# Kernel optimization log

Measured on AMD Instinct MI355X. Metric: run time of the kernel, lower is better.

The kernel has to match this reference:

```python
import jax, jax.numpy as jnp
import numpy as np

N = 100000      # nodes
E = 1600000     # edges (before self-loops)
F_IN = 512      # input features
H = 8           # heads layer 1
D = 8           # per-head dim layer 1
C = 40          # classes (layer 2 out, heads=1)
NEG_SLOPE = 0.2 # PyG GATConv default negative_slope


def setup_inputs() -> dict:
    key = jax.random.key(0)
    ks = jax.random.split(key, 10)
    x = jax.random.normal(ks[0], (N, F_IN), jnp.float32)
    edge_index = jax.random.randint(ks[1], (2, E), 0, N, dtype=jnp.int32)
    W1 = jax.random.normal(ks[2], (F_IN, H * D), jnp.float32) / np.float32(np.sqrt(F_IN))
    att_src1 = jax.random.normal(ks[3], (H, D), jnp.float32) / np.float32(np.sqrt(D))
    att_dst1 = jax.random.normal(ks[4], (H, D), jnp.float32) / np.float32(np.sqrt(D))
    b1 = jnp.zeros((H * D,), jnp.float32)
    W2 = jax.random.normal(ks[5], (H * D, C), jnp.float32) / np.float32(np.sqrt(H * D))
    att_src2 = jax.random.normal(ks[6], (1, C), jnp.float32) / np.float32(np.sqrt(C))
    att_dst2 = jax.random.normal(ks[7], (1, C), jnp.float32) / np.float32(np.sqrt(C))
    b2 = jnp.zeros((C,), jnp.float32)
    return {"x": x, "edge_index": edge_index, "W1": W1, "att_src1": att_src1,
            "att_dst1": att_dst1, "b1": b1, "W2": W2, "att_src2": att_src2,
            "att_dst2": att_dst2, "b2": b2}


def _gat_layer(x, src, dst, W, a_src, a_dst, heads, dim):
    # Dense projection, then per-head attention logits.
    h = (x @ W).reshape(-1, heads, dim)            # [N, H, D]
    alpha_s = jnp.einsum('nhd,hd->nh', h, a_src)   # [N, H]
    alpha_d = jnp.einsum('nhd,hd->nh', h, a_dst)
    e = jax.nn.leaky_relu(alpha_s[src] + alpha_d[dst], NEG_SLOPE)  # [E, H]
    # Segment softmax over edges grouped by destination node.
    emax = jax.ops.segment_max(e, dst, num_segments=N)
    emax = jnp.where(jnp.isfinite(emax), emax, 0.0)
    ee = jnp.exp(e - emax[dst])
    denom = jax.ops.segment_sum(ee, dst, num_segments=N)
    alpha = ee / (denom[dst] + 1e-16)              # [E, H]
    # Scatter-aggregate weighted neighbor features.
    msg = h[src] * alpha[:, :, None]               # [E, H, D]
    return jax.ops.segment_sum(msg, dst, num_segments=N)  # [N, H, D]


def reference(x, edge_index, W1, att_src1, att_dst1, b1, W2, att_src2, att_dst2, b2):
    # PyG GATConv adds self-loops by default.
    loops = jnp.arange(N, dtype=edge_index.dtype)
    src = jnp.concatenate([edge_index[0], loops])
    dst = jnp.concatenate([edge_index[1], loops])
    # Layer 1: 8 heads, concat=True, then ELU. (dropouts identity in eval mode)
    h1 = _gat_layer(x, src, dst, W1, att_src1, att_dst1, H, D).reshape(N, H * D) + b1
    h1 = jax.nn.elu(h1)
    # Layer 2: 1 head, concat=False -> mean over heads (trivial for H=1).
    h2 = _gat_layer(h1, src, dst, W2, att_src2, att_dst2, 1, C)[:, 0, :] + b2
    return jax.nn.log_softmax(h2, axis=1)
```

## Files before the change

kernel.cpp:

```cpp
#include <hip/hip_runtime.h>

#define F_IN   512
#define HD     64
#define NHEAD  8
#define NC     40
#define NEG    0.2f

typedef __attribute__((ext_vector_type(8))) short bf16x8;
typedef __attribute__((ext_vector_type(4))) float f32x4;

__device__ __forceinline__ float lrelu(float x) { return x > 0.0f ? x : NEG * x; }

__device__ __forceinline__ short f2bf(float f) {
    unsigned u = __float_as_uint(f);
    u += 0x7FFF + ((u >> 16) & 1);
    return (short)(u >> 16);
}
__device__ __forceinline__ float bf2f(short h) {
    return __uint_as_float(((unsigned)(unsigned short)h) << 16);
}
__device__ __forceinline__ float bfl(unsigned u) { return __uint_as_float(u << 16); }
__device__ __forceinline__ float bfh(unsigned u) { return __uint_as_float(u & 0xFFFF0000u); }

__global__ void zero_kernel(int* __restrict__ p, int n) {
    int i = blockIdx.x * 256 + threadIdx.x;
    if (i < n) p[i] = 0;
}

__global__ __launch_bounds__(256) void scanA_kernel(const int* __restrict__ deg,
                                                    int* __restrict__ incl,
                                                    int* __restrict__ bsum, int Nn) {
    __shared__ int wsum[4];
    int t = threadIdx.x, b = blockIdx.x;
    int base = b * 1024 + t * 4;
    int v0 = (base + 0) < Nn ? deg[base + 0] : 0;
    int v1 = (base + 1) < Nn ? deg[base + 1] : 0;
    int v2 = (base + 2) < Nn ? deg[base + 2] : 0;
    int v3 = (base + 3) < Nn ? deg[base + 3] : 0;
    int p0 = v0, p1 = p0 + v1, p2 = p1 + v2, p3 = p2 + v3;
    int lane = t & 63, w = t >> 6;
    int sc = p3;
    for (int off = 1; off < 64; off <<= 1) {
        int u = __shfl_up(sc, off);
        if (lane >= off) sc += u;
    }
    if (lane == 63) wsum[w] = sc;
    __syncthreads();
    int woff = 0;
#pragma unroll
    for (int i = 0; i < 4; ++i) if (i < w) woff += wsum[i];
    int excl = woff + sc - p3;
    if (base + 0 < Nn) incl[base + 0] = excl + p0;
    if (base + 1 < Nn) incl[base + 1] = excl + p1;
    if (base + 2 < Nn) incl[base + 2] = excl + p2;
    if (base + 3 < Nn) incl[base + 3] = excl + p3;
    if (t == 0) bsum[b] = wsum[0] + wsum[1] + wsum[2] + wsum[3];
}

__global__ void scanB_kernel(int* __restrict__ bsum, int nb) {
    int lane = threadIdx.x;
    int a = lane < nb ? bsum[lane] : 0;
    int c = (lane + 64) < nb ? bsum[lane + 64] : 0;
    int sa = a, sc2 = c;
    for (int off = 1; off < 64; off <<= 1) {
        int u = __shfl_up(sa, off);  if (lane >= off) sa += u;
        int u2 = __shfl_up(sc2, off); if (lane >= off) sc2 += u2;
    }
    int totA = __shfl(sa, 63);
    int ea = sa - a;
    int ec = totA + sc2 - c;
    if (lane < nb) bsum[lane] = ea;
    if (lane + 64 < nb) bsum[lane + 64] = ec;
}

__global__ void scanC_kernel(const int* __restrict__ incl, const int* __restrict__ bsum,
                             int* __restrict__ rp, int Nn) {
    int i = blockIdx.x * 256 + threadIdx.x;
    if (i == 0) rp[0] = 0;
    if (i < Nn) rp[i + 1] = incl[i] + bsum[i >> 10];
}

__global__ void scatter_kernel(const int* __restrict__ src, const int* __restrict__ dst,
                               const int* __restrict__ pos, const int* __restrict__ rp,
                               int* __restrict__ col, int E) {
    int e = blockIdx.x * 256 + threadIdx.x;
    if (e < E) {
        int d = dst[e];
        col[rp[d] + pos[e]] = src[e];
    }
}

__global__ void wsplit_kernel(const float* __restrict__ W, short* __restrict__ Whp,
                              short* __restrict__ Wlp) {
    int t = blockIdx.x * 256 + threadIdx.x;
    if (t >= F_IN * HD) return;
    int k = t >> 6, c = t & 63;
    float wv = W[t];
    short hh = f2bf(wv);
    int idx = (((k >> 3) * 64 + c) << 3) + (k & 7);
    Whp[idx] = hh;
    Wlp[idx] = f2bf(wv - bf2f(hh));
}

#define G1_BM 64
__global__ __launch_bounds__(256) void g1c_kernel(const float* __restrict__ X,
                                                  const short* __restrict__ Whp,
                                                  const short* __restrict__ Wlp,
                                                  const float* __restrict__ att_s,
                                                  const float* __restrict__ att_d,
                                                  unsigned short* __restrict__ Hp,
                                                  float* __restrict__ as1,
                                                  float* __restrict__ ad1,
                                                  const int* __restrict__ dst,
                                                  int* __restrict__ deg,
                                                  int* __restrict__ pos,
                                                  int Nn, int E, int nG1) {
    int tid = threadIdx.x;

    if ((int)blockIdx.x >= nG1) {
        int e = ((int)blockIdx.x - nG1) * 256 + tid;
        if (e < E) pos[e] = atomicAdd(&deg[dst[e]], 1);
        return;
    }

    int wid = tid >> 6, lane = tid & 63;
    int lrow = lane & 15, kgrp = lane >> 4;
    int row0 = blockIdx.x * G1_BM;
    int rowA = row0 + wid * 16 + lrow;

    float ats[4], atd[4];
#pragma unroll
    for (int fc = 0; fc < 4; ++fc) { ats[fc] = att_s[fc * 16 + lrow]; atd[fc] = att_d[fc * 16 + lrow]; }

    f32x4 acc[4];
#pragma unroll
    for (int fc = 0; fc < 4; ++fc) acc[fc] = (f32x4){0.f, 0.f, 0.f, 0.f};

    bool valid = rowA < Nn;
    const float* xrow = X + (size_t)rowA * F_IN + kgrp * 8;
    const bf16x8* WhV = reinterpret_cast<const bf16x8*>(Whp);
    const bf16x8* WlV = reinterpret_cast<const bf16x8*>(Wlp);

    float4 a_cur[2], a_nxt[2];
    if (valid) {
        a_cur[0] = *reinterpret_cast<const float4*>(xrow);
        a_cur[1] = *reinterpret_cast<const float4*>(xrow + 4);
    } else {
        a_cur[0] = a_cur[1] = make_float4(0.f, 0.f, 0.f, 0.f);
    }

#pragma unroll 2
    for (int it = 0; it < F_IN / 32; ++it) {
        if (it + 1 < F_IN / 32) {
            if (valid) {
                const float* p = xrow + (it + 1) * 32;
                a_nxt[0] = *reinterpret_cast<const float4*>(p);
                a_nxt[1] = *reinterpret_cast<const float4*>(p + 4);
            } else {
                a_nxt[0] = a_nxt[1] = make_float4(0.f, 0.f, 0.f, 0.f);
            }
        }
        bf16x8 af;
        {
            float fs[8] = {a_cur[0].x, a_cur[0].y, a_cur[0].z, a_cur[0].w,
                           a_cur[1].x, a_cur[1].y, a_cur[1].z, a_cur[1].w};
#pragma unroll
            for (int j = 0; j < 8; ++j) af[j] = f2bf(fs[j]);
        }
        const bf16x8* bhp = WhV + (size_t)(it * 4 + kgrp) * 64;
        const bf16x8* blp = WlV + (size_t)(it * 4 + kgrp) * 64;
#pragma unroll
        for (int fc = 0; fc < 4; ++fc) {
            bf16x8 bh = bhp[fc * 16 + lrow];
            bf16x8 bl = blp[fc * 16 + lrow];
            acc[fc] = __builtin_amdgcn_mfma_f32_16x16x32_bf16(af, bh, acc[fc], 0, 0, 0);
            acc[fc] = __builtin_amdgcn_mfma_f32_16x16x32_bf16(af, bl, acc[fc], 0, 0, 0);
        }
        a_cur[0] = a_nxt[0];
        a_cur[1] = a_nxt[1];
    }

#pragma unroll
    for (int r = 0; r < 4; ++r) {
        int gr = row0 + wid * 16 + kgrp * 4 + r;
        float hv[4], sp[4], dp[4];
#pragma unroll
        for (int fc = 0; fc < 4; ++fc) {
            hv[fc] = acc[fc][r];
            sp[fc] = hv[fc] * ats[fc];
            dp[fc] = hv[fc] * atd[fc];
        }
#pragma unroll
        for (int mask = 1; mask <= 4; mask <<= 1) {
#pragma unroll
            for (int fc = 0; fc < 4; ++fc) {
                sp[fc] += __shfl_xor(sp[fc], mask);
                dp[fc] += __shfl_xor(dp[fc], mask);
            }
        }
        if (gr < Nn) {
#pragma unroll
            for (int fc = 0; fc < 4; ++fc)
                Hp[(size_t)gr * HD + fc * 16 + lrow] = (unsigned short)f2bf(hv[fc]);
            if ((lane & 7) == 0) {
                int hh = lrow >> 3;
#pragma unroll
                for (int fc = 0; fc < 4; ++fc) {
                    as1[gr * NHEAD + fc * 2 + hh] = sp[fc];
                    ad1[gr * NHEAD + fc * 2 + hh] = dp[fc];
                }
            }
        }
    }
}

__global__ __launch_bounds__(256) void agg1_kernel(const unsigned short* __restrict__ Hp,
                                                   const float* __restrict__ as1,
                                                   const float* __restrict__ ad1,
                                                   const int* __restrict__ col,
                                                   const int* __restrict__ rp,
                                                   const float* __restrict__ b1,
                                                   float* __restrict__ h1, int Nn) {
    int n = blockIdx.x * 4 + (threadIdx.x >> 6);
    int lane = threadIdx.x & 63;
    if (n >= Nn) return;
    int slot = lane >> 3, j = lane & 7;
    int beg = rp[n], end = rp[n + 1];
    float adv1 = ad1[n * NHEAD + j];
    float acc[8] = {0, 0, 0, 0, 0, 0, 0, 0};
    float dw = 0.f;
    for (int t = beg + slot; t < end; t += 8) {
        int s = col[t];
        float w = __expf(lrelu(as1[s * NHEAD + j] + adv1));
        dw += w;
        uint4 u = *reinterpret_cast<const uint4*>(&Hp[(size_t)s * HD + j * 8]);
        acc[0] += w * bfl(u.x); acc[1] += w * bfh(u.x);
        acc[2] += w * bfl(u.y); acc[3] += w * bfh(u.y);
        acc[4] += w * bfl(u.z); acc[5] += w * bfh(u.z);
        acc[6] += w * bfl(u.w); acc[7] += w * bfh(u.w);
    }
#pragma unroll
    for (int mask = 8; mask < 64; mask <<= 1) {
#pragma unroll
        for (int i = 0; i < 8; ++i) acc[i] += __shfl_xor(acc[i], mask);
        dw += __shfl_xor(dw, mask);
    }
    float w = __expf(lrelu(as1[n * NHEAD + j] + adv1));
    uint4 u = *reinterpret_cast<const uint4*>(&Hp[(size_t)n * HD + j * 8]);
    acc[0] += w * bfl(u.x); acc[1] += w * bfh(u.x);
    acc[2] += w * bfl(u.y); acc[3] += w * bfh(u.y);
    acc[4] += w * bfl(u.z); acc[5] += w * bfh(u.z);
    acc[6] += w * bfl(u.w); acc[7] += w * bfh(u.w);
    dw += w;
    float invd = 1.0f / (dw + 1e-16f);
    float4 b0 = *reinterpret_cast<const float4*>(&b1[j * 8]);
    float4 b4 = *reinterpret_cast<const float4*>(&b1[j * 8 + 4]);
    float bb[8] = {b0.x, b0.y, b0.z, b0.w, b4.x, b4.y, b4.z, b4.w};
#pragma unroll
    for (int i = 0; i < 8; ++i) {
        float v = acc[i] * invd + bb[i];
        acc[i] = v > 0.0f ? v : __expf(v) - 1.0f;
    }
    if (slot == 0) {
        float4 o0 = make_float4(acc[0], acc[1], acc[2], acc[3]);
        float4 o1 = make_float4(acc[4], acc[5], acc[6], acc[7]);
        *reinterpret_cast<float4*>(&h1[(size_t)n * HD + j * 8]) = o0;
        *reinterpret_cast<float4*>(&h1[(size_t)n * HD + j * 8 + 4]) = o1;
    }
}

#define G2R 64
__global__ __launch_bounds__(256) void gemm2_kernel(const float* __restrict__ H1,
                                                    const float* __restrict__ W2,
                                                    const float* __restrict__ asw,
                                                    const float* __restrict__ adw,
                                                    unsigned int* __restrict__ h2p,
                                                    float* __restrict__ as2,
                                                    float* __restrict__ ad2, int Nn) {
    __shared__ float Hs[G2R][HD + 1];
    __shared__ float W2s[HD][NC];
    __shared__ float asv[NC], adv[NC];
    int tid = threadIdx.x;
    for (int i = tid; i < HD * NC; i += 256) W2s[i / NC][i % NC] = W2[i];
    if (tid < NC) { asv[tid] = asw[tid]; adv[tid] = adw[tid]; }
    int row0 = blockIdx.x * G2R;
#pragma unroll
    for (int i = 0; i < 4; ++i) {
        int linear = i * 1024 + tid * 4;
        int r = linear >> 6, c = linear & 63;
        int gr = row0 + r;
        float4 v = make_float4(0.f, 0.f, 0.f, 0.f);
        if (gr < Nn) v = *reinterpret_cast<const float4*>(&H1[(size_t)gr * HD + c]);
        Hs[r][c + 0] = v.x; Hs[r][c + 1] = v.y; Hs[r][c + 2] = v.z; Hs[r][c + 3] = v.w;
    }
    __syncthreads();
    int row = tid >> 2, cg = tid & 3;
    int gr = row0 + row;
    float acc[10];
#pragma unroll
    for (int jj = 0; jj < 10; ++jj) acc[jj] = 0.0f;
    for (int k = 0; k < HD; ++k) {
        float a = Hs[row][k];
#pragma unroll
        for (int jj = 0; jj < 10; ++jj) acc[jj] += a * W2s[k][cg * 10 + jj];
    }
    float sa = 0.0f, da = 0.0f;
#pragma unroll
    for (int jj = 0; jj < 10; ++jj) {
        sa += acc[jj] * asv[cg * 10 + jj];
        da += acc[jj] * adv[cg * 10 + jj];
    }
    sa += __shfl_xor(sa, 1); sa += __shfl_xor(sa, 2);
    da += __shfl_xor(da, 1); da += __shfl_xor(da, 2);
    if (gr < Nn) {
        if (cg == 0) { as2[gr] = sa; ad2[gr] = da; }
#pragma unroll
        for (int jj = 0; jj < 5; ++jj) {
            unsigned int u = ((unsigned int)(unsigned short)f2bf(acc[2 * jj + 1]) << 16) |
                             (unsigned short)f2bf(acc[2 * jj]);
            h2p[(size_t)gr * 20 + cg * 5 + jj] = u;
        }
    }
}

__global__ __launch_bounds__(256) void agg2_kernel(const unsigned int* __restrict__ h2p,
                                                   const float* __restrict__ as2,
                                                   const float* __restrict__ ad2,
                                                   const int* __restrict__ col,
                                                   const int* __restrict__ rp,
                                                   const float* __restrict__ b2,
                                                   float* __restrict__ out, int Nn) {
    int n = blockIdx.x * 4 + (threadIdx.x >> 6);
    int lane = threadIdx.x & 63;
    if (n >= Nn) return;
    int slot = lane >> 4, l16 = lane & 15;
    bool act = l16 < 10;
    int beg = rp[n], end = rp[n + 1];
    float adv = ad2[n];
    float4 acc = make_float4(0.f, 0.f, 0.f, 0.f);
    float dw = 0.f;
    for (int t = beg + slot; t < end; t += 4) {
        int s = col[t];
        float w = __expf(lrelu(as2[s] + adv));
        dw += w;
        if (act) {
            uint2 u = *reinterpret_cast<const uint2*>(&h2p[(size_t)s * 20 + l16 * 2]);
            acc.x += w * bfl(u.x); acc.y += w * bfh(u.x);
            acc.z += w * bfl(u.y); acc.w += w * bfh(u.y);
        }
    }
#pragma unroll
    for (int mask = 16; mask < 64; mask <<= 1) {
        acc.x += __shfl_xor(acc.x, mask);
        acc.y += __shfl_xor(acc.y, mask);
        acc.z += __shfl_xor(acc.z, mask);
        acc.w += __shfl_xor(acc.w, mask);
        dw    += __shfl_xor(dw, mask);
    }
    float w = __expf(lrelu(as2[n] + adv));
    dw += w;
    float invd = 1.0f / (dw + 1e-16f);
    if (act) {
        uint2 u = *reinterpret_cast<const uint2*>(&h2p[(size_t)n * 20 + l16 * 2]);
        float4 bb = *reinterpret_cast<const float4*>(&b2[l16 * 4]);
        acc.x = (acc.x + w * bfl(u.x)) * invd + bb.x;
        acc.y = (acc.y + w * bfh(u.x)) * invd + bb.y;
        acc.z = (acc.z + w * bfl(u.y)) * invd + bb.z;
        acc.w = (acc.w + w * bfh(u.y)) * invd + bb.w;
    }
    float mloc = act ? fmaxf(fmaxf(acc.x, acc.y), fmaxf(acc.z, acc.w)) : -INFINITY;
#pragma unroll
    for (int mask = 1; mask < 16; mask <<= 1) mloc = fmaxf(mloc, __shfl_xor(mloc, mask));
    float s4 = act ? (__expf(acc.x - mloc) + __expf(acc.y - mloc) +
                      __expf(acc.z - mloc) + __expf(acc.w - mloc)) : 0.0f;
#pragma unroll
    for (int mask = 1; mask < 16; mask <<= 1) s4 += __shfl_xor(s4, mask);
    float lse = mloc + __logf(s4);
    if (slot == 0 && act) {
        float4 o = make_float4(acc.x - lse, acc.y - lse, acc.z - lse, acc.w - lse);
        *reinterpret_cast<float4*>(&out[(size_t)n * NC + l16 * 4]) = o;
    }
}

extern "C" void kernel_launch(void* const* d_in, const int* in_sizes, int n_in,
                              void* d_out, int out_size, void* d_ws, size_t ws_size,
                              hipStream_t stream) {
    const float* x    = (const float*)d_in[0];
    const int*   ei   = (const int*)d_in[1];
    const float* W1   = (const float*)d_in[2];
    const float* as1w = (const float*)d_in[3];
    const float* ad1w = (const float*)d_in[4];
    const float* b1   = (const float*)d_in[5];
    const float* W2   = (const float*)d_in[6];
    const float* as2w = (const float*)d_in[7];
    const float* ad2w = (const float*)d_in[8];
    const float* b2   = (const float*)d_in[9];
    float* out = (float*)d_out;

    int Nn = in_sizes[0] / F_IN;
    int E  = in_sizes[1] / 2;
    const int* srcv = ei;
    const int* dstv = ei + E;

    char* ws = (char*)d_ws;
    size_t off = 0;
    auto alloc = [&](size_t bytes) { size_t cur = off; off += (bytes + 255) & ~255ULL; return cur; };
    unsigned short* Hp = (unsigned short*)(ws + alloc((size_t)Nn * HD * 2));
    float* h1   = (float*)(ws + alloc((size_t)Nn * HD * 4));
    float* as1v = (float*)(ws + alloc((size_t)Nn * NHEAD * 4));
    float* ad1v = (float*)(ws + alloc((size_t)Nn * NHEAD * 4));
    unsigned int* h2p = (unsigned int*)(ws + alloc((size_t)Nn * 20 * 4));
    float* as2v = (float*)(ws + alloc((size_t)Nn * 4));
    float* ad2v = (float*)(ws + alloc((size_t)Nn * 4));
    int* deg  = (int*)(ws + alloc((size_t)Nn * 4));
    int* incl = (int*)(ws + alloc((size_t)Nn * 4));
    int* rp   = (int*)(ws + alloc((size_t)(Nn + 1) * 4));
    int* pos  = (int*)(ws + alloc((size_t)E * 4));
    int* col  = (int*)(ws + alloc((size_t)E * 4));
    int* bsum = (int*)(ws + alloc(256 * 4));
    short* Whp = (short*)(ws + alloc((size_t)F_IN * HD * 2));
    short* Wlp = (short*)(ws + alloc((size_t)F_IN * HD * 2));

    int nb   = (Nn + 1023) / 1024;
    int nG1  = (Nn + G1_BM - 1) / G1_BM;
    int nCNT = (E + 255) / 256;

    zero_kernel<<<(Nn + 255) / 256, 256, 0, stream>>>(deg, Nn);
    wsplit_kernel<<<(F_IN * HD + 255) / 256, 256, 0, stream>>>(W1, Whp, Wlp);
    g1c_kernel<<<nG1 + nCNT, 256, 0, stream>>>(x, Whp, Wlp, as1w, ad1w, Hp, as1v, ad1v,
                                               dstv, deg, pos, Nn, E, nG1);
    scanA_kernel<<<nb, 256, 0, stream>>>(deg, incl, bsum, Nn);
    scanB_kernel<<<1, 64, 0, stream>>>(bsum, nb);
    scanC_kernel<<<(Nn + 255) / 256, 256, 0, stream>>>(incl, bsum, rp, Nn);
    scatter_kernel<<<(E + 255) / 256, 256, 0, stream>>>(srcv, dstv, pos, rp, col, E);

    agg1_kernel<<<(Nn + 3) / 4, 256, 0, stream>>>(Hp, as1v, ad1v, col, rp, b1, h1, Nn);
    gemm2_kernel<<<(Nn + G2R - 1) / G2R, 256, 0, stream>>>(h1, W2, as2w, ad2w, h2p, as2v, ad2v, Nn);
    agg2_kernel<<<(Nn + 3) / 4, 256, 0, stream>>>(h2p, as2v, ad2v, col, rp, b2, out, Nn);
}
```

Baseline: 351.4 us.

## Drop bf16 hi/lo weight split and stage W1 tiles in LDS double buffer

The layer-1 projection previously ran two bf16 MFMAs per tile, one for the high part of W1 and one for the residual low part, to approximate fp32 weights. It now converts W1 to a single bf16 copy, halving the MFMA count and the weight reads. W tiles are also staged through a double-buffered shared-memory array, loaded cooperatively per 64-wide K chunk, instead of being read from global memory by every wave. This costs precision on the weights and adds block-wide barriers each iteration; the kernel is probably bound by reading X, so the gain may be limited.

New measurement: 366.3 us. 1.04x slower.

```diff
diff --git a/kernel.cpp b/kernel.cpp
--- a/kernel.cpp
+++ b/kernel.cpp
@@ -90,22 +90,16 @@
     }
 }
 
-__global__ void wsplit_kernel(const float* __restrict__ W, short* __restrict__ Whp,
-                              short* __restrict__ Wlp) {
+__global__ void wconv_kernel(const float* __restrict__ W, short* __restrict__ Whp) {
     int t = blockIdx.x * 256 + threadIdx.x;
     if (t >= F_IN * HD) return;
     int k = t >> 6, c = t & 63;
-    float wv = W[t];
-    short hh = f2bf(wv);
-    int idx = (((k >> 3) * 64 + c) << 3) + (k & 7);
-    Whp[idx] = hh;
-    Wlp[idx] = f2bf(wv - bf2f(hh));
+    Whp[((((k >> 3) * 64 + c)) << 3) + (k & 7)] = f2bf(W[t]);
 }
 
 #define G1_BM 64
 __global__ __launch_bounds__(256) void g1c_kernel(const float* __restrict__ X,
                                                   const short* __restrict__ Whp,
-                                                  const short* __restrict__ Wlp,
                                                   const float* __restrict__ att_s,
                                                   const float* __restrict__ att_d,
                                                   unsigned short* __restrict__ Hp,
@@ -115,6 +109,7 @@
                                                   int* __restrict__ deg,
                                                   int* __restrict__ pos,
                                                   int Nn, int E, int nG1) {
+    __shared__ short Bs[2][4096];
     int tid = threadIdx.x;
 
     if ((int)blockIdx.x >= nG1) {
@@ -138,46 +133,56 @@
 
     bool valid = rowA < Nn;
     const float* xrow = X + (size_t)rowA * F_IN + kgrp * 8;
-    const bf16x8* WhV = reinterpret_cast<const bf16x8*>(Whp);
-    const bf16x8* WlV = reinterpret_cast<const bf16x8*>(Wlp);
-
-    float4 a_cur[2], a_nxt[2];
-    if (valid) {
-        a_cur[0] = *reinterpret_cast<const float4*>(xrow);
-        a_cur[1] = *reinterpret_cast<const float4*>(xrow + 4);
-    } else {
-        a_cur[0] = a_cur[1] = make_float4(0.f, 0.f, 0.f, 0.f);
-    }
-
-#pragma unroll 2
-    for (int it = 0; it < F_IN / 32; ++it) {
-        if (it + 1 < F_IN / 32) {
-            if (valid) {
-                const float* p = xrow + (it + 1) * 32;
-                a_nxt[0] = *reinterpret_cast<const float4*>(p);
-                a_nxt[1] = *reinterpret_cast<const float4*>(p + 4);
-            } else {
-                a_nxt[0] = a_nxt[1] = make_float4(0.f, 0.f, 0.f, 0.f);
+    const uint4* Wg = reinterpret_cast<const uint4*>(Whp);
+    const float4 z4 = make_float4(0.f, 0.f, 0.f, 0.f);
+
+    {
+        uint4* Bv = reinterpret_cast<uint4*>(&Bs[0][0]);
+        Bv[tid] = Wg[tid];
+        Bv[tid + 256] = Wg[tid + 256];
+    }
+    float4 ac[2][2], an[2][2];
+#pragma unroll
+    for (int kb = 0; kb < 2; ++kb) {
+        ac[kb][0] = valid ? *reinterpret_cast<const float4*>(xrow + kb * 32)     : z4;
+        ac[kb][1] = valid ? *reinterpret_cast<const float4*>(xrow + kb * 32 + 4) : z4;
+    }
+    __syncthreads();
+
+#pragma unroll
+    for (int it = 0; it < F_IN / 64; ++it) {
+        if (it + 1 < F_IN / 64) {
+            uint4* Bv = reinterpret_cast<uint4*>(&Bs[(it + 1) & 1][0]);
+            const uint4* Wt = Wg + (size_t)(it + 1) * 512;
+            Bv[tid] = Wt[tid];
+            Bv[tid + 256] = Wt[tid + 256];
+#pragma unroll
+            for (int kb = 0; kb < 2; ++kb) {
+                const float* p = xrow + (it + 1) * 64 + kb * 32;
+                an[kb][0] = valid ? *reinterpret_cast<const float4*>(p)     : z4;
+                an[kb][1] = valid ? *reinterpret_cast<const float4*>(p + 4) : z4;
             }
         }
-        bf16x8 af;
-        {
-            float fs[8] = {a_cur[0].x, a_cur[0].y, a_cur[0].z, a_cur[0].w,
-                           a_cur[1].x, a_cur[1].y, a_cur[1].z, a_cur[1].w};
+#pragma unroll
+        for (int kb = 0; kb < 2; ++kb) {
+            float fs[8] = {ac[kb][0].x, ac[kb][0].y, ac[kb][0].z, ac[kb][0].w,
+                           ac[kb][1].x, ac[kb][1].y, ac[kb][1].z, ac[kb][1].w};
+            bf16x8 af;
 #pragma unroll
             for (int j = 0; j < 8; ++j) af[j] = f2bf(fs[j]);
-        }
-        const bf16x8* bhp = WhV + (size_t)(it * 4 + kgrp) * 64;
-        const bf16x8* blp = WlV + (size_t)(it * 4 + kgrp) * 64;
-#pragma unroll
-        for (int fc = 0; fc < 4; ++fc) {
-            bf16x8 bh = bhp[fc * 16 + lrow];
-            bf16x8 bl = blp[fc * 16 + lrow];
-            acc[fc] = __builtin_amdgcn_mfma_f32_16x16x32_bf16(af, bh, acc[fc], 0, 0, 0);
-            acc[fc] = __builtin_amdgcn_mfma_f32_16x16x32_bf16(af, bl, acc[fc], 0, 0, 0);
-        }
-        a_cur[0] = a_nxt[0];
-        a_cur[1] = a_nxt[1];
+#pragma unroll
+            for (int fc = 0; fc < 4; ++fc) {
+                bf16x8 b = *reinterpret_cast<const bf16x8*>(
+                    &Bs[it & 1][(((kb * 4 + kgrp) * 64) + fc * 16 + lrow) * 8]);
+                acc[fc] = __builtin_amdgcn_mfma_f32_16x16x32_bf16(af, b, acc[fc], 0, 0, 0);
+            }
+        }
+        __syncthreads();
+#pragma unroll
+        for (int kb = 0; kb < 2; ++kb) {
+            ac[kb][0] = an[kb][0];
+            ac[kb][1] = an[kb][1];
+        }
     }
 
 #pragma unroll
@@ -419,15 +424,14 @@
     int* col  = (int*)(ws + alloc((size_t)E * 4));
     int* bsum = (int*)(ws + alloc(256 * 4));
     short* Whp = (short*)(ws + alloc((size_t)F_IN * HD * 2));
-    short* Wlp = (short*)(ws + alloc((size_t)F_IN * HD * 2));
 
     int nb   = (Nn + 1023) / 1024;
     int nG1  = (Nn + G1_BM - 1) / G1_BM;
     int nCNT = (E + 255) / 256;
 
     zero_kernel<<<(Nn + 255) / 256, 256, 0, stream>>>(deg, Nn);
-    wsplit_kernel<<<(F_IN * HD + 255) / 256, 256, 0, stream>>>(W1, Whp, Wlp);
-    g1c_kernel<<<nG1 + nCNT, 256, 0, stream>>>(x, Whp, Wlp, as1w, ad1w, Hp, as1v, ad1v,
+    wconv_kernel<<<(F_IN * HD + 255) / 256, 256, 0, stream>>>(W1, Whp);
+    g1c_kernel<<<nG1 + nCNT, 256, 0, stream>>>(x, Whp, as1w, ad1w, Hp, as1v, ad1v,
                                                dstv, deg, pos, Nn, E, nG1);
     scanA_kernel<<<nb, 256, 0, stream>>>(deg, incl, bsum, Nn);
     scanB_kernel<<<1, 64, 0, stream>>>(bsum, nb);
```
